# Kernel tuning notes

Hardware: AMD Instinct MI355X
Metric: run time of the kernel (lower is better)

## Reference

```python
import jax, jax.numpy as jnp
import numpy as np


def setup_inputs() -> dict:
    key = jax.random.key(0)
    k1, k2, k3 = jax.random.split(key, 3)
    B, N, F, D = 8, 2048, 512, 512
    x = jax.random.normal(k1, (B, N, F), dtype=jnp.float32)
    a = jax.random.uniform(k2, (B, N, N), dtype=jnp.float32)
    kernel = jax.random.normal(k3, (F, D), dtype=jnp.float32) * (1.0 / np.sqrt(F))
    return {"x": x, "a": a, "kernel": kernel}


def reference(x, a, kernel):
    # t = a @ x : [B,N,N] x [B,N,F] -> [B,N,F]
    t = jnp.einsum('bnm,bmf->bnf', a, x)
    # feature transform: [B,N,F] x [F,D] -> [B,N,D]
    out = jnp.einsum('bnf,fd->bnd', t, kernel)
    # dropout is inference-mode (identity); no bias
    out = jax.nn.relu(out)
    # padded mask: zero rows of x produce zero outputs
    mask = (jnp.sum((x != 0).astype(jnp.float32), axis=-1, keepdims=True) > 0).astype(jnp.float32)
    return out * mask
```

## Files before the change

kernel.cpp:

```cpp
#include <hip/hip_runtime.h>

typedef __bf16 bf16x8 __attribute__((ext_vector_type(8)));
typedef float f32x4 __attribute__((ext_vector_type(4)));
typedef unsigned int u32x4 __attribute__((ext_vector_type(4)));

__device__ __forceinline__ unsigned short f2bf(float f) {
  unsigned u = __builtin_bit_cast(unsigned, f);
  u += 0x7FFFu + ((u >> 16) & 1u);
  return (unsigned short)(u >> 16);
}

__device__ __forceinline__ void gl2lds16(const void* g, void* l) {
  __builtin_amdgcn_global_load_lds((const __attribute__((address_space(1))) void*)g,
                                   (__attribute__((address_space(3))) void*)l, 16, 0, 0);
}

__device__ __forceinline__ bf16x8 cvt8v(f32x4 a, f32x4 b) {
  bf16x8 r;
  r[0] = (__bf16)a[0]; r[1] = (__bf16)a[1]; r[2] = (__bf16)a[2]; r[3] = (__bf16)a[3];
  r[4] = (__bf16)b[0]; r[5] = (__bf16)b[1]; r[6] = (__bf16)b[2]; r[7] = (__bf16)b[3];
  return r;
}

__global__ void transpose_cvt(const float* __restrict__ in, unsigned short* __restrict__ out) {
  __shared__ float tile[32][33];
  const int r0 = blockIdx.x * 32, c0 = blockIdx.y * 32;
  const int tx = threadIdx.x, ty = threadIdx.y;
#pragma unroll
  for (int i = 0; i < 4; ++i) tile[ty + i * 8][tx] = in[(size_t)(r0 + ty + i * 8) * 512 + c0 + tx];
  __syncthreads();
#pragma unroll
  for (int i = 0; i < 4; ++i) {
    const int cc = ty + i * 8;
    out[(size_t)(c0 + cc) * 512 + r0 + tx] = f2bf(tile[tx][cc]);
  }
}

__global__ __launch_bounds__(512, 1) void gemm_y(const float* __restrict__ A0,
                                                 const unsigned short* __restrict__ B0,
                                                 unsigned short* __restrict__ yT,
                                                 int* __restrict__ mask) {
  constexpr int APITCH = 512, BPITCH = 512, NT = 16;
  __shared__ __align__(16) char lds[131072];
  const int bid = blockIdx.x;
  const int mt = bid >> 1, nt = bid & 1;
  const int b = mt >> 4, m0 = (mt & 15) * 128, n0 = nt * 256;
  const float* Ab = A0 + ((size_t)b * 2048 + m0) * APITCH;
  const unsigned short* Bb = B0 + (size_t)n0 * BPITCH;

  const int tid = threadIdx.x, w = tid >> 6, L = tid & 63;
  const int wr = w >> 2, wc = w & 3, r = L & 15, hi = L >> 4;

  const char* aSrc = (const char*)(Ab + (size_t)(w * 16 + r) * APITCH + hi * 4);
  const char* bSrc0 = (const char*)(Bb + (size_t)(w * 32 + r) * BPITCH + hi * 8);
  const char* bSrc1 = (const char*)(Bb + (size_t)(w * 32 + 16 + r) * BPITCH + hi * 8);

  int aro[4], bro[4];
#pragma unroll
  for (int mi = 0; mi < 4; ++mi)
    aro[mi] = (((wr * 4 + mi) * 2 + (hi >> 1)) << 10) + ((hi & 1) << 9) + r * 16;
#pragma unroll
  for (int ni = 0; ni < 4; ++ni) bro[ni] = 16384 + ((wc * 4 + ni) << 10) + L * 16;

  f32x4 acc[4][4] = {};
  unsigned anz[4] = {0u, 0u, 0u, 0u};

#define STAGE(SLOT, TA)                                                          \
  {                                                                              \
    char* ls = lds + (SLOT) * 32768;                                             \
    gl2lds16(aSrc + (size_t)(TA) * 128, ls + ((w * 2 + 0) << 10));               \
    gl2lds16(aSrc + (size_t)(TA) * 128 + 64, ls + ((w * 2 + 1) << 10));          \
    gl2lds16(bSrc0 + (size_t)(TA) * 64, ls + 16384 + ((w * 2 + 0) << 10));       \
    gl2lds16(bSrc1 + (size_t)(TA) * 64, ls + 16384 + ((w * 2 + 1) << 10));       \
  }

  STAGE(0, 0)
  STAGE(1, 1)
  STAGE(2, 2)
  asm volatile("s_waitcnt vmcnt(8)" ::: "memory");
  __builtin_amdgcn_sched_barrier(0);
  __builtin_amdgcn_s_barrier();
  __builtin_amdgcn_sched_barrier(0);

#pragma unroll 1
  for (int t = 0; t < NT; ++t) {
    const int slot = (t + 3) & 3, cur = t & 3;
    const int ta = (t + 3 < NT) ? (t + 3) : (NT - 1);
    STAGE(slot, ta)
    __builtin_amdgcn_sched_barrier(0);
    const char* cb = lds + cur * 32768;

    bf16x8 bfr[4];
#pragma unroll
    for (int ni = 0; ni < 4; ++ni) bfr[ni] = *(const bf16x8*)(cb + bro[ni]);
    f32x4 lo0 = *(const f32x4*)(cb + aro[0]), hh0 = *(const f32x4*)(cb + aro[0] + 256);
    f32x4 lo1 = *(const f32x4*)(cb + aro[1]), hh1 = *(const f32x4*)(cb + aro[1] + 256);
    asm volatile("s_waitcnt lgkmcnt(0)" ::: "memory");
    __builtin_amdgcn_sched_barrier(0);
    if (wc == 0) {
      u32x4 u0 = __builtin_bit_cast(u32x4, lo0), u1 = __builtin_bit_cast(u32x4, hh0);
      anz[0] |= (u0[0] | u0[1] | u0[2] | u0[3] | u1[0] | u1[1] | u1[2] | u1[3]) & 0x7fffffffu;
      u32x4 v0 = __builtin_bit_cast(u32x4, lo1), v1 = __builtin_bit_cast(u32x4, hh1);
      anz[1] |= (v0[0] | v0[1] | v0[2] | v0[3] | v1[0] | v1[1] | v1[2] | v1[3]) & 0x7fffffffu;
    }
    bf16x8 af0 = cvt8v(lo0, hh0), af1 = cvt8v(lo1, hh1);
    __builtin_amdgcn_s_setprio(1);
#pragma unroll
    for (int ni = 0; ni < 4; ++ni)
      acc[0][ni] = __builtin_amdgcn_mfma_f32_16x16x32_bf16(af0, bfr[ni], acc[0][ni], 0, 0, 0);
#pragma unroll
    for (int ni = 0; ni < 4; ++ni)
      acc[1][ni] = __builtin_amdgcn_mfma_f32_16x16x32_bf16(af1, bfr[ni], acc[1][ni], 0, 0, 0);
    __builtin_amdgcn_s_setprio(0);

    f32x4 lo2 = *(const f32x4*)(cb + aro[2]), hh2 = *(const f32x4*)(cb + aro[2] + 256);
    f32x4 lo3 = *(const f32x4*)(cb + aro[3]), hh3 = *(const f32x4*)(cb + aro[3] + 256);
    asm volatile("s_waitcnt lgkmcnt(0)" ::: "memory");
    __builtin_amdgcn_sched_barrier(0);
    if (wc == 0) {
      u32x4 u0 = __builtin_bit_cast(u32x4, lo2), u1 = __builtin_bit_cast(u32x4, hh2);
      anz[2] |= (u0[0] | u0[1] | u0[2] | u0[3] | u1[0] | u1[1] | u1[2] | u1[3]) & 0x7fffffffu;
      u32x4 v0 = __builtin_bit_cast(u32x4, lo3), v1 = __builtin_bit_cast(u32x4, hh3);
      anz[3] |= (v0[0] | v0[1] | v0[2] | v0[3] | v1[0] | v1[1] | v1[2] | v1[3]) & 0x7fffffffu;
    }
    bf16x8 af2 = cvt8v(lo2, hh2), af3 = cvt8v(lo3, hh3);
    __builtin_amdgcn_s_setprio(1);
#pragma unroll
    for (int ni = 0; ni < 4; ++ni)
      acc[2][ni] = __builtin_amdgcn_mfma_f32_16x16x32_bf16(af2, bfr[ni], acc[2][ni], 0, 0, 0);
#pragma unroll
    for (int ni = 0; ni < 4; ++ni)
      acc[3][ni] = __builtin_amdgcn_mfma_f32_16x16x32_bf16(af3, bfr[ni], acc[3][ni], 0, 0, 0);
    __builtin_amdgcn_s_setprio(0);

    asm volatile("s_waitcnt vmcnt(8)" ::: "memory");
    __builtin_amdgcn_sched_barrier(0);
    __builtin_amdgcn_s_barrier();
    __builtin_amdgcn_sched_barrier(0);
  }
  asm volatile("s_waitcnt vmcnt(0)" ::: "memory");
#undef STAGE

  if (wc == 0) {
#pragma unroll
    for (int mi = 0; mi < 4; ++mi) {
      unsigned v = anz[mi];
      v |= __shfl_xor(v, 16);
      v |= __shfl_xor(v, 32);
      if (hi == 0) mask[b * 2048 + m0 + wr * 64 + mi * 16 + r] = (v != 0u) ? 1 : 0;
    }
  }
#pragma unroll
  for (int mi = 0; mi < 4; ++mi)
#pragma unroll
    for (int ni = 0; ni < 4; ++ni) {
      const int col = n0 + wc * 64 + ni * 16 + r;
      const int nrow = m0 + wr * 64 + mi * 16 + hi * 4;
      ushort4 s;
      s.x = f2bf(acc[mi][ni][0]);
      s.y = f2bf(acc[mi][ni][1]);
      s.z = f2bf(acc[mi][ni][2]);
      s.w = f2bf(acc[mi][ni][3]);
      *(ushort4*)(yT + (((size_t)b * 512 + col) << 11) + nrow) = s;
    }
}

template <int APITCH, int BPITCH, int NT>
__global__ __launch_bounds__(512, 1) void gemm_big2(const float* __restrict__ A0,
                                                    const unsigned short* __restrict__ B0,
                                                    const int* __restrict__ mask,
                                                    float* __restrict__ out) {
  __shared__ __align__(16) char lds[122880];

  const int bid = blockIdx.x;
  const int b = bid & 7, mt = bid >> 3;
  const int m0 = mt * 64;
  const float* Ab = A0 + ((size_t)b * 2048 + m0) * APITCH;
  const unsigned short* Bb = B0 + (size_t)b * 512 * BPITCH;

  const int tid = threadIdx.x, w = tid >> 6, L = tid & 63;
  const int wr = w >> 2, wc = w & 3, r = L & 15, hi = L >> 4;

  const char* aSrc =
      (const char*)(Ab + (size_t)((w >> 1) * 16 + r) * APITCH) + (w & 1) * 64 + hi * 16;

  const char* bSrc[4];
#pragma unroll
  for (int j = 0; j < 4; ++j)
    bSrc[j] = (const char*)(Bb + (size_t)((w * 4 + j) * 16 + r) * BPITCH) + hi * 16;

  int aro[2];
#pragma unroll
  for (int mi = 0; mi < 2; ++mi)
    aro[mi] = (((wr * 2 + mi) * 2 + (hi >> 1)) << 10) + ((hi & 1) << 9) + r * 16;
  int bro[8];
#pragma unroll
  for (int ni = 0; ni < 8; ++ni) bro[ni] = 8192 + ((wc * 8 + ni) << 10) + L * 16;

  f32x4 acc[2][8] = {};

#define STAGE(SLOT, TA)                                                       \
  {                                                                           \
    char* ls = lds + (SLOT) * 40960;                                          \
    gl2lds16(aSrc + (size_t)(TA) * 128, ls + (w << 10));                      \
    _Pragma("unroll") for (int j = 0; j < 4; ++j)                             \
        gl2lds16(bSrc[j] + (size_t)(TA) * 64, ls + 8192 + ((w * 4 + j) << 10)); \
  }

  STAGE(0, 0)
  STAGE(1, 1)
  asm volatile("s_waitcnt vmcnt(5)" ::: "memory");
  __builtin_amdgcn_sched_barrier(0);
  __builtin_amdgcn_s_barrier();
  __builtin_amdgcn_sched_barrier(0);

#pragma unroll 1
  for (int t = 0; t < NT; ++t) {
    const int slot = (t + 2) % 3;
    const int ta = (t + 2 < NT) ? (t + 2) : (NT - 1);
    STAGE(slot, ta)
    __builtin_amdgcn_sched_barrier(0);

    const char* cb = lds + (t % 3) * 40960;
    bf16x8 bfr[8];
#pragma unroll
    for (int ni = 0; ni < 8; ++ni) bfr[ni] = *(const bf16x8*)(cb + bro[ni]);
    f32x4 lo0 = *(const f32x4*)(cb + aro[0]), hh0 = *(const f32x4*)(cb + aro[0] + 256);
    f32x4 lo1 = *(const f32x4*)(cb + aro[1]), hh1 = *(const f32x4*)(cb + aro[1] + 256);
    asm volatile("s_waitcnt lgkmcnt(0)" ::: "memory");
    __builtin_amdgcn_sched_barrier(0);
    bf16x8 af0 = cvt8v(lo0, hh0), af1 = cvt8v(lo1, hh1);
    __builtin_amdgcn_s_setprio(1);
#pragma unroll
    for (int ni = 0; ni < 8; ++ni)
      acc[0][ni] = __builtin_amdgcn_mfma_f32_16x16x32_bf16(af0, bfr[ni], acc[0][ni], 0, 0, 0);
#pragma unroll
    for (int ni = 0; ni < 8; ++ni)
      acc[1][ni] = __builtin_amdgcn_mfma_f32_16x16x32_bf16(af1, bfr[ni], acc[1][ni], 0, 0, 0);
    __builtin_amdgcn_s_setprio(0);

    asm volatile("s_waitcnt vmcnt(5)" ::: "memory");
    __builtin_amdgcn_sched_barrier(0);
    __builtin_amdgcn_s_barrier();
    __builtin_amdgcn_sched_barrier(0);
  }
  asm volatile("s_waitcnt vmcnt(0)" ::: "memory");
#undef STAGE

  const int* mrow = mask + b * 2048 + m0 + wr * 32;
#pragma unroll
  for (int mi = 0; mi < 2; ++mi) {
    const int4 mv = *(const int4*)(mrow + mi * 16 + hi * 4);
    const int mvv[4] = {mv.x, mv.y, mv.z, mv.w};
#pragma unroll
    for (int ni = 0; ni < 8; ++ni) {
      const int col = wc * 128 + ni * 16 + r;
      float* op = out + (size_t)(b * 2048 + m0 + wr * 32 + mi * 16 + hi * 4) * 512 + col;
#pragma unroll
      for (int rr = 0; rr < 4; ++rr) {
        float v = fmaxf(acc[mi][ni][rr], 0.0f);
        if (mvv[rr] == 0) v = 0.0f;
        op[(size_t)rr * 512] = v;
      }
    }
  }
}

extern "C" void kernel_launch(void* const* d_in, const int* in_sizes, int n_in,
                              void* d_out, int out_size, void* d_ws, size_t ws_size,
                              hipStream_t stream) {
  const float* x = (const float*)d_in[0];
  const float* a = (const float*)d_in[1];
  const float* wk = (const float*)d_in[2];
  float* out = (float*)d_out;

  char* ws = (char*)d_ws;
  unsigned short* wT = (unsigned short*)ws;
  unsigned short* yT = (unsigned short*)(ws + (1u << 19));
  int* mask = (int*)(ws + (1u << 19) + (16u << 20));

  transpose_cvt<<<dim3(16, 16), dim3(32, 8), 0, stream>>>(wk, wT);
  gemm_y<<<256, 512, 0, stream>>>(x, wT, yT, mask);
  gemm_big2<2048, 2048, 64><<<256, 512, 0, stream>>>(a, yT, mask, out);
}
```

Before: 113.4 us.

## Warp-specialize big GEMM into producer/consumer waves with LDS flag ring

Replaces the barrier-synchronized triple-buffered GEMM with a warp-specialized kernel. Four waves load A/B tiles into a 4-slot LDS ring, signalling readiness with shared-memory counters, and four waves run MFMAs on a 128x256 tile. The intent is to decouple loads from compute and remove block-wide barriers. The new tiling splits the output columns across two blocks, so the large fp32 adjacency matrix is fetched twice, and spin-waiting on LDS flags adds overhead.

```diff
diff --git a/kernel.cpp b/kernel.cpp
--- a/kernel.cpp
+++ b/kernel.cpp
@@ -165,97 +165,113 @@
     }
 }
 
-template <int APITCH, int BPITCH, int NT>
-__global__ __launch_bounds__(512, 1) void gemm_big2(const float* __restrict__ A0,
-                                                    const unsigned short* __restrict__ B0,
-                                                    const int* __restrict__ mask,
-                                                    float* __restrict__ out) {
-  __shared__ __align__(16) char lds[122880];
+template <int NT>
+__global__ __launch_bounds__(512, 1) void gemm_pc(const float* __restrict__ a,
+                                                  const unsigned short* __restrict__ yT,
+                                                  const int* __restrict__ mask,
+                                                  float* __restrict__ out) {
+  __shared__ __align__(16) char slots[4][32768];
+  __shared__ int rdy[4];
+  __shared__ int done[4];
 
   const int bid = blockIdx.x;
-  const int b = bid & 7, mt = bid >> 3;
-  const int m0 = mt * 64;
-  const float* Ab = A0 + ((size_t)b * 2048 + m0) * APITCH;
-  const unsigned short* Bb = B0 + (size_t)b * 512 * BPITCH;
+  const int b = bid & 7, idx = bid >> 3;
+  const int m0 = (idx & 15) * 128, n0 = (idx >> 4) * 256;
+  const float* Ab = a + ((size_t)b * 2048 + m0) * 2048;
+  const unsigned short* Bb = yT + ((size_t)b * 512 + n0) * 2048;
 
   const int tid = threadIdx.x, w = tid >> 6, L = tid & 63;
-  const int wr = w >> 2, wc = w & 3, r = L & 15, hi = L >> 4;
-
-  const char* aSrc =
-      (const char*)(Ab + (size_t)((w >> 1) * 16 + r) * APITCH) + (w & 1) * 64 + hi * 16;
-
-  const char* bSrc[4];
-#pragma unroll
-  for (int j = 0; j < 4; ++j)
-    bSrc[j] = (const char*)(Bb + (size_t)((w * 4 + j) * 16 + r) * BPITCH) + hi * 16;
-
-  int aro[2];
-#pragma unroll
-  for (int mi = 0; mi < 2; ++mi)
-    aro[mi] = (((wr * 2 + mi) * 2 + (hi >> 1)) << 10) + ((hi & 1) << 9) + r * 16;
-  int bro[8];
-#pragma unroll
-  for (int ni = 0; ni < 8; ++ni) bro[ni] = 8192 + ((wc * 8 + ni) << 10) + L * 16;
-
-  f32x4 acc[2][8] = {};
-
-#define STAGE(SLOT, TA)                                                       \
-  {                                                                           \
-    char* ls = lds + (SLOT) * 40960;                                          \
-    gl2lds16(aSrc + (size_t)(TA) * 128, ls + (w << 10));                      \
-    _Pragma("unroll") for (int j = 0; j < 4; ++j)                             \
-        gl2lds16(bSrc[j] + (size_t)(TA) * 64, ls + 8192 + ((w * 4 + j) << 10)); \
-  }
-
-  STAGE(0, 0)
-  STAGE(1, 1)
-  asm volatile("s_waitcnt vmcnt(5)" ::: "memory");
-  __builtin_amdgcn_sched_barrier(0);
-  __builtin_amdgcn_s_barrier();
-  __builtin_amdgcn_sched_barrier(0);
+  const int r = L & 15, hi = L >> 4;
+
+  if (tid < 4) { rdy[tid] = 0; done[tid] = 0; }
+  __syncthreads();
+
+  volatile int* vrdy = rdy;
+  volatile int* vdone = done;
+
+  if (w >= 4) {
+    const int p = w - 4;
+    const char* aS[4];
+    const char* bS[4];
+#pragma unroll
+    for (int j = 0; j < 4; ++j) {
+      const int g = p * 4 + j;
+      aS[j] = (const char*)Ab + ((size_t)((g >> 1) * 16 + r) * 2048) * 4 + hi * 16 + (g & 1) * 64;
+      bS[j] = (const char*)Bb + ((size_t)(g * 16 + r) * 2048) * 2 + hi * 16;
+    }
+#pragma unroll 1
+    for (int t = 0; t < NT; ++t) {
+      const int s = t & 3;
+      const int gt = (t >> 2) * 4;
+      while (vdone[s] < gt) __builtin_amdgcn_s_sleep(1);
+      asm volatile("" ::: "memory");
+      __builtin_amdgcn_sched_barrier(0);
+      char* sb = slots[s];
+#pragma unroll
+      for (int j = 0; j < 4; ++j) {
+        const int g = p * 4 + j;
+        gl2lds16(aS[j] + (size_t)t * 128, sb + (g << 10));
+        gl2lds16(bS[j] + (size_t)t * 64, sb + 16384 + (g << 10));
+      }
+      asm volatile("s_waitcnt vmcnt(0)" ::: "memory");
+      __builtin_amdgcn_sched_barrier(0);
+      if (L == 0) atomicAdd(&rdy[s], 1);
+    }
+    return;
+  }
+
+  const int wr = w >> 1, wc = w & 1;
+  int aro[4], bro[8];
+#pragma unroll
+  for (int mi = 0; mi < 4; ++mi)
+    aro[mi] = (((wr * 4 + mi) * 2 + (hi >> 1)) << 10) + ((hi & 1) << 9) + r * 16;
+#pragma unroll
+  for (int ni = 0; ni < 8; ++ni) bro[ni] = 16384 + ((wc * 8 + ni) << 10) + L * 16;
+
+  f32x4 acc[4][8] = {};
 
 #pragma unroll 1
   for (int t = 0; t < NT; ++t) {
-    const int slot = (t + 2) % 3;
-    const int ta = (t + 2 < NT) ? (t + 2) : (NT - 1);
-    STAGE(slot, ta)
-    __builtin_amdgcn_sched_barrier(0);
-
-    const char* cb = lds + (t % 3) * 40960;
+    const int s = t & 3;
+    const int target = ((t >> 2) + 1) * 4;
+    while (vrdy[s] < target) __builtin_amdgcn_s_sleep(1);
+    asm volatile("" ::: "memory");
+    __builtin_amdgcn_sched_barrier(0);
+    const char* sb = slots[s];
+
     bf16x8 bfr[8];
 #pragma unroll
-    for (int ni = 0; ni < 8; ++ni) bfr[ni] = *(const bf16x8*)(cb + bro[ni]);
-    f32x4 lo0 = *(const f32x4*)(cb + aro[0]), hh0 = *(const f32x4*)(cb + aro[0] + 256);
-    f32x4 lo1 = *(const f32x4*)(cb + aro[1]), hh1 = *(const f32x4*)(cb + aro[1] + 256);
+    for (int ni = 0; ni < 8; ++ni) bfr[ni] = *(const bf16x8*)(sb + bro[ni]);
+    f32x4 lo[4], hh[4];
+#pragma unroll
+    for (int mi = 0; mi < 4; ++mi) {
+      lo[mi] = *(const f32x4*)(sb + aro[mi]);
+      hh[mi] = *(const f32x4*)(sb + aro[mi] + 256);
+    }
     asm volatile("s_waitcnt lgkmcnt(0)" ::: "memory");
     __builtin_amdgcn_sched_barrier(0);
-    bf16x8 af0 = cvt8v(lo0, hh0), af1 = cvt8v(lo1, hh1);
+    if (L == 0) atomicAdd(&done[s], 1);
+    bf16x8 af[4];
+#pragma unroll
+    for (int mi = 0; mi < 4; ++mi) af[mi] = cvt8v(lo[mi], hh[mi]);
     __builtin_amdgcn_s_setprio(1);
 #pragma unroll
-    for (int ni = 0; ni < 8; ++ni)
-      acc[0][ni] = __builtin_amdgcn_mfma_f32_16x16x32_bf16(af0, bfr[ni], acc[0][ni], 0, 0, 0);
-#pragma unroll
-    for (int ni = 0; ni < 8; ++ni)
-      acc[1][ni] = __builtin_amdgcn_mfma_f32_16x16x32_bf16(af1, bfr[ni], acc[1][ni], 0, 0, 0);
+    for (int mi = 0; mi < 4; ++mi)
+#pragma unroll
+      for (int ni = 0; ni < 8; ++ni)
+        acc[mi][ni] = __builtin_amdgcn_mfma_f32_16x16x32_bf16(af[mi], bfr[ni], acc[mi][ni], 0, 0, 0);
     __builtin_amdgcn_s_setprio(0);
-
-    asm volatile("s_waitcnt vmcnt(5)" ::: "memory");
-    __builtin_amdgcn_sched_barrier(0);
-    __builtin_amdgcn_s_barrier();
-    __builtin_amdgcn_sched_barrier(0);
-  }
-  asm volatile("s_waitcnt vmcnt(0)" ::: "memory");
-#undef STAGE
-
-  const int* mrow = mask + b * 2048 + m0 + wr * 32;
-#pragma unroll
-  for (int mi = 0; mi < 2; ++mi) {
+  }
+
+  const int* mrow = mask + b * 2048 + m0 + wr * 64;
+#pragma unroll
+  for (int mi = 0; mi < 4; ++mi) {
     const int4 mv = *(const int4*)(mrow + mi * 16 + hi * 4);
     const int mvv[4] = {mv.x, mv.y, mv.z, mv.w};
 #pragma unroll
     for (int ni = 0; ni < 8; ++ni) {
-      const int col = wc * 128 + ni * 16 + r;
-      float* op = out + (size_t)(b * 2048 + m0 + wr * 32 + mi * 16 + hi * 4) * 512 + col;
+      const int col = n0 + wc * 128 + ni * 16 + r;
+      float* op = out + (size_t)(b * 2048 + m0 + wr * 64 + mi * 16 + hi * 4) * 512 + col;
 #pragma unroll
       for (int rr = 0; rr < 4; ++rr) {
         float v = fmaxf(acc[mi][ni][rr], 0.0f);
@@ -281,5 +297,5 @@
 
   transpose_cvt<<<dim3(16, 16), dim3(32, 8), 0, stream>>>(wk, wT);
   gemm_y<<<256, 512, 0, stream>>>(x, wT, yT, mask);
-  gemm_big2<2048, 2048, 64><<<256, 512, 0, stream>>>(a, yT, mask, out);
-}
+  gemm_pc<64><<<256, 512, 0, stream>>>(a, yT, mask, out);
+}
```

New measurement: 102.1 us. 10.0% less time.
